# Kernel tuning notes

Measured on AMD Instinct MI355X. Metric: run time of the kernel, lower is better.

## Reference

```python
import jax, jax.numpy as jnp
import numpy as np

VOCAB, EMB, HID, OUT = 128, 128, 256, 2
B, T = 128, 2048


def setup_inputs() -> dict:
    key = jax.random.key(0)
    ks = jax.random.split(key, 8)
    s_ih = 1.0 / np.sqrt(HID)
    inp = {
        "x": jax.random.randint(ks[0], (B, T), 0, VOCAB, dtype=jnp.int32),
        "emb": jax.random.normal(ks[1], (VOCAB, EMB), jnp.float32),
        "W_ih": jax.random.uniform(ks[2], (4 * HID, EMB), jnp.float32, -s_ih, s_ih),
        "W_hh": jax.random.uniform(ks[3], (4 * HID, HID), jnp.float32, -s_ih, s_ih),
        "b_ih": jax.random.uniform(ks[4], (4 * HID,), jnp.float32, -s_ih, s_ih),
        "b_hh": jax.random.uniform(ks[5], (4 * HID,), jnp.float32, -s_ih, s_ih),
        "fc_W": jax.random.normal(ks[6], (OUT, HID), jnp.float32) * np.sqrt(6.0 / (HID + OUT)),
        "fc_b": jnp.zeros((OUT,), jnp.float32),
    }
    return inp


def _lstm_last_hidden(xe, W_ih, W_hh, b_ih, b_hh):
    # xe: [B, T, E]. Precompute all input-to-hidden gate projections (batched GEMM).
    Bsz = xe.shape[0]
    H = W_hh.shape[1]
    xg = jnp.einsum('bte,ge->tbg', xe, W_ih) + (b_ih + b_hh)  # [T, B, 4H]

    def step(carry, xt):
        h, c = carry
        g = xt + h @ W_hh.T                 # [B, 4H]
        i, f, gg, o = jnp.split(g, 4, axis=-1)  # PyTorch gate order i,f,g,o
        i = jax.nn.sigmoid(i)
        f = jax.nn.sigmoid(f)
        gg = jnp.tanh(gg)
        o = jax.nn.sigmoid(o)
        c = f * c + i * gg
        h = o * jnp.tanh(c)
        return (h, c), None

    h0 = jnp.zeros((Bsz, H), xe.dtype)
    c0 = jnp.zeros((Bsz, H), xe.dtype)
    (hT, _), _ = jax.lax.scan(step, (h0, c0), xg)
    return hT  # == output[:, -1, :] for a uni-directional LSTM


def reference(x, emb, W_ih, W_hh, b_ih, b_hh, fc_W, fc_b):
    xe = emb[x]                                   # [B, T, E] embedding lookup
    hT = _lstm_last_hidden(xe, W_ih, W_hh, b_ih, b_hh)
    logits = hT @ fc_W.T + fc_b                   # [B, OUT]
    return logits
```

## Files before the change

### kernel.cpp

```cpp
#include <hip/hip_runtime.h>

#define T_LEN 2048
#define HID   256
#define G4    1024
#define EMBD  128
#define VOCAB 128
#define OUTC  2
#define BSUB  2
#define NWG   64
#define CHK   64
#define XCHS  72
#define HSB   288
#define LOG2E 1.44269504088896340736f

typedef int   i32x4 __attribute__((ext_vector_type(4)));
typedef float f32x4 __attribute__((ext_vector_type(4)));

__device__ __align__(16) float Pbuf[VOCAB * G4];
__device__ __align__(16) signed char Wqb[G4 * HID];
__device__ float Winv[G4];

__global__ void build_P(const float* __restrict__ emb, const float* __restrict__ W_ih,
                        const float* __restrict__ b_ih, const float* __restrict__ b_hh) {
    const int v = blockIdx.x >> 2;
    const int c = ((blockIdx.x & 3) << 8) + threadIdx.x;
    __shared__ float es[EMBD];
    if (threadIdx.x < EMBD) es[threadIdx.x] = emb[v * EMBD + threadIdx.x];
    __syncthreads();
    const float* wr = W_ih + c * EMBD;
    float acc = 0.f;
    #pragma unroll 8
    for (int e = 0; e < EMBD; ++e) acc += es[e] * wr[e];
    const float ks = ((c >> 8) == 2) ? (-2.f * LOG2E) : (-LOG2E);
    const int g  = c >> 8;
    const int rr = c & 255;
    const int wi = rr >> 5;
    const int nt = (rr >> 4) & 1;
    const int l  = rr & 15;
    Pbuf[v * G4 + wi * 128 + nt * 64 + l * 4 + g] = (acc + b_ih[c] + b_hh[c]) * ks;
}

__global__ void quant_W(const float* __restrict__ W_hh) {
    const int row = blockIdx.x;
    const int k   = threadIdx.x;
    __shared__ float red[4];
    const float wv = W_hh[row * HID + k];
    float a = fabsf(wv);
    #pragma unroll
    for (int o = 32; o > 0; o >>= 1) a = fmaxf(a, __shfl_down(a, o, 64));
    if ((k & 63) == 0) red[k >> 6] = a;
    __syncthreads();
    const float m = fmaxf(fmaxf(fmaxf(red[0], red[1]), red[2]), fmaxf(red[3], 1e-30f));
    Wqb[row * HID + k] = (signed char)(int)rintf(wv * (127.f / m));
    const float ks = ((row >> 8) == 2) ? (-2.f * LOG2E) : (-LOG2E);
    if (k == 0) Winv[row] = m * (1.f / (127.f * 127.f)) * ks;
}

__device__ __forceinline__ float sig_p(float p) {
    return __builtin_amdgcn_rcpf(1.f + __builtin_amdgcn_exp2f(p));
}

__global__ __launch_bounds__(512, 2) void lstm_chain(
        const int* __restrict__ x, const float* __restrict__ fc_W,
        const float* __restrict__ fc_b, float* __restrict__ out) {
    __shared__ __align__(16) signed char habuf[2][BSUB * HSB];
    __shared__ int   xch[BSUB * XCHS];
    __shared__ float hfin[BSUB * HID];

    const int tid  = threadIdx.x;
    const int w    = tid >> 6;
    const int lane = tid & 63;
    const int l15  = lane & 15;
    const int quad = lane >> 4;
    const int bbase = blockIdx.x * BSUB;
    const int ub    = w * 32;
    const int bq    = quad >> 1;
    const int ntq   = quad & 1;
    const int colq  = ub + ntq * 16 + l15;

    i32x4 Bf[2][4][4];
    #pragma unroll
    for (int nt = 0; nt < 2; ++nt)
        #pragma unroll
        for (int g = 0; g < 4; ++g) {
            const signed char* wr = Wqb + (size_t)(g * HID + ub + nt * 16 + l15) * HID;
            #pragma unroll
            for (int kt = 0; kt < 4; ++kt)
                Bf[nt][g][kt] = *(const i32x4*)(wr + kt * 64 + quad * 16);
        }
    float winvv[4];
    #pragma unroll
    for (int g = 0; g < 4; ++g) winvv[g] = Winv[g * HID + colq];

    if (tid < BSUB * HSB / 4) ((int*)habuf[0])[tid] = 0;

    float cst = 0.f;
    f32x4 xga, xgb;
    const i32x4 zero4 = {0, 0, 0, 0};
    const float* pbase = Pbuf + w * 128 + ntq * 64 + l15 * 4;
    const signed char* habA = habuf[0] + (l15 >> 3) * HSB + quad * 16;
    const signed char* habB = habuf[1] + (l15 >> 3) * HSB + quad * 16;

#define GATHER(TT, XG)                                                        \
    {                                                                         \
        const int xv = xch[bq * XCHS + (TT)];                                 \
        XG = *(const f32x4*)(pbase + (size_t)xv * G4);                        \
    }

#define STEP(HAB, HN, XC, XN, PF, TT, TCUR)                                   \
    {                                                                         \
        i32x4 af[4];                                                          \
        _Pragma("unroll")                                                     \
        for (int kt = 0; kt < 4; ++kt)                                        \
            af[kt] = *(const i32x4*)((HAB) + kt * 64);                        \
        if (PF) GATHER((TT), XN);                                             \
        i32x4 a0[4], a1[4];                                                   \
        _Pragma("unroll")                                                     \
        for (int g = 0; g < 4; ++g)                                           \
            a0[g] = __builtin_amdgcn_mfma_i32_16x16x64_i8(af[0], Bf[0][g][0], zero4, 0, 0, 0); \
        _Pragma("unroll")                                                     \
        for (int kt = 1; kt < 4; ++kt)                                        \
            _Pragma("unroll")                                                 \
            for (int g = 0; g < 4; ++g)                                       \
                a0[g] = __builtin_amdgcn_mfma_i32_16x16x64_i8(af[kt], Bf[0][g][kt], a0[g], 0, 0, 0); \
        _Pragma("unroll")                                                     \
        for (int g = 0; g < 4; ++g)                                           \
            a1[g] = __builtin_amdgcn_mfma_i32_16x16x64_i8(af[0], Bf[1][g][0], zero4, 0, 0, 0); \
        _Pragma("unroll")                                                     \
        for (int kt = 1; kt < 4; ++kt)                                        \
            _Pragma("unroll")                                                 \
            for (int g = 0; g < 4; ++g)                                       \
                a1[g] = __builtin_amdgcn_mfma_i32_16x16x64_i8(af[kt], Bf[1][g][kt], a1[g], 0, 0, 0); \
                         \
        const int gi_ = ntq ? a1[0][0] : a0[0][0];                            \
        const int gf_ = ntq ? a1[1][0] : a0[1][0];                            \
        const int gg_ = ntq ? a1[2][0] : a0[2][0];                            \
        const int go_ = ntq ? a1[3][0] : a0[3][0];                            \
        const float is = sig_p(fmaf((float)gi_, winvv[0], XC[0]));            \
        const float fs = sig_p(fmaf((float)gf_, winvv[1], XC[1]));            \
        const float gt = fmaf(2.f, sig_p(fmaf((float)gg_, winvv[2], XC[2])), -1.f); \
        const float os = sig_p(fmaf((float)go_, winvv[3], XC[3]));            \
        const float c  = fmaf(fs, cst, is * gt);                              \
        cst = c;                                                              \
        const float hq = fmaf(254.f, sig_p(c * (-2.f * LOG2E)), -127.f) * os; \
        (HN)[bq * HSB + colq] = (signed char)(int)rintf(hq);                  \
        if ((TCUR) == T_LEN - 1) hfin[bq * HID + colq] = hq * (1.f / 127.f);  \
        __syncthreads();                                                      \
    }

    #pragma unroll 1
    for (int ch = 0; ch < T_LEN / CHK; ++ch) {
        if (tid < BSUB * CHK)
            xch[(tid >> 6) * XCHS + (tid & 63)] =
                x[(bbase + (tid >> 6)) * T_LEN + ch * CHK + (tid & 63)];
        __syncthreads();
        GATHER(0, xga);
        const int tb = ch * CHK;
        #pragma unroll 1
        for (int tt = 0; tt < CHK; tt += 2) {
            STEP(habA, habuf[1], xga, xgb, 1, tt + 1, tb + tt);
            STEP(habB, habuf[0], xgb, xga, (tt < CHK - 2), tt + 2, tb + tt + 1);
        }
    }
#undef STEP
#undef GATHER

    if (tid < BSUB * OUTC) {
        const int b = tid >> 1, o = tid & 1;
        float s = fc_b[o];
        #pragma unroll 8
        for (int j = 0; j < HID; ++j) s += hfin[b * HID + j] * fc_W[o * HID + j];
        out[(bbase + b) * OUTC + o] = s;
    }
}

extern "C" void kernel_launch(void* const* d_in, const int* in_sizes, int n_in,
                              void* d_out, int out_size, void* d_ws, size_t ws_size,
                              hipStream_t stream) {
    const int*   x    = (const int*)  d_in[0];
    const float* emb  = (const float*)d_in[1];
    const float* W_ih = (const float*)d_in[2];
    const float* W_hh = (const float*)d_in[3];
    const float* b_ih = (const float*)d_in[4];
    const float* b_hh = (const float*)d_in[5];
    const float* fc_W = (const float*)d_in[6];
    const float* fc_b = (const float*)d_in[7];
    float* out = (float*)d_out;
    (void)d_ws; (void)ws_size;

    build_P<<<dim3(VOCAB * 4), dim3(256), 0, stream>>>(emb, W_ih, b_ih, b_hh);
    quant_W<<<dim3(G4), dim3(HID), 0, stream>>>(W_hh);
    lstm_chain<<<dim3(NWG), dim3(512), 0, stream>>>(x, fc_W, fc_b, out);
}
```

Measured before the change: 1.408 ms.

## Preload full token sequence to LDS and overlap gate math with second MFMA set

Loads each block's whole token sequence (2x2048 ints) into shared memory once at kernel start, removing the per-64-step chunk reloads and their extra barriers. The step now computes gate nonlinearities for the first MFMA tile right after its accumulation, before issuing the second tile's MFMAs, so the transcendental work can overlap MFMA latency. Both tiles' gates are then computed and selected, doubling the activation ALU work per lane and adding register pressure plus 16KB of LDS.

```diff
diff --git a/kernel.cpp b/kernel.cpp
--- a/kernel.cpp
+++ b/kernel.cpp
@@ -8,8 +8,6 @@
 #define OUTC  2
 #define BSUB  2
 #define NWG   64
-#define CHK   64
-#define XCHS  72
 #define HSB   288
 #define LOG2E 1.44269504088896340736f
 
@@ -64,7 +62,7 @@
         const int* __restrict__ x, const float* __restrict__ fc_W,
         const float* __restrict__ fc_b, float* __restrict__ out) {
     __shared__ __align__(16) signed char habuf[2][BSUB * HSB];
-    __shared__ int   xch[BSUB * XCHS];
+    __shared__ __align__(16) int xls[BSUB][T_LEN];
     __shared__ float hfin[BSUB * HID];
 
     const int tid  = threadIdx.x;
@@ -92,6 +90,12 @@
     #pragma unroll
     for (int g = 0; g < 4; ++g) winvv[g] = Winv[g * HID + colq];
 
+    {
+        const i32x4* xsrc = (const i32x4*)(x + (size_t)bbase * T_LEN);
+        i32x4* xdst = (i32x4*)xls;
+        xdst[tid]       = xsrc[tid];
+        xdst[tid + 512] = xsrc[tid + 512];
+    }
     if (tid < BSUB * HSB / 4) ((int*)habuf[0])[tid] = 0;
 
     float cst = 0.f;
@@ -103,7 +107,7 @@
 
 #define GATHER(TT, XG)                                                        \
     {                                                                         \
-        const int xv = xch[bq * XCHS + (TT)];                                 \
+        const int xv = xls[bq][(TT)];                                         \
         XG = *(const f32x4*)(pbase + (size_t)xv * G4);                        \
     }
 
@@ -123,6 +127,12 @@
             _Pragma("unroll")                                                 \
             for (int g = 0; g < 4; ++g)                                       \
                 a0[g] = __builtin_amdgcn_mfma_i32_16x16x64_i8(af[kt], Bf[0][g][kt], a0[g], 0, 0, 0); \
+          \
+        const float i0 = sig_p(fmaf((float)a0[0][0], winvv[0], XC[0]));       \
+        const float f0 = sig_p(fmaf((float)a0[1][0], winvv[1], XC[1]));       \
+        const float g0 = fmaf(2.f, sig_p(fmaf((float)a0[2][0], winvv[2], XC[2])), -1.f); \
+        const float o0 = sig_p(fmaf((float)a0[3][0], winvv[3], XC[3]));       \
+        const float ig0 = i0 * g0;                                            \
         _Pragma("unroll")                                                     \
         for (int g = 0; g < 4; ++g)                                           \
             a1[g] = __builtin_amdgcn_mfma_i32_16x16x64_i8(af[0], Bf[1][g][0], zero4, 0, 0, 0); \
@@ -131,16 +141,16 @@
             _Pragma("unroll")                                                 \
             for (int g = 0; g < 4; ++g)                                       \
                 a1[g] = __builtin_amdgcn_mfma_i32_16x16x64_i8(af[kt], Bf[1][g][kt], a1[g], 0, 0, 0); \
-                         \
-        const int gi_ = ntq ? a1[0][0] : a0[0][0];                            \
-        const int gf_ = ntq ? a1[1][0] : a0[1][0];                            \
-        const int gg_ = ntq ? a1[2][0] : a0[2][0];                            \
-        const int go_ = ntq ? a1[3][0] : a0[3][0];                            \
-        const float is = sig_p(fmaf((float)gi_, winvv[0], XC[0]));            \
-        const float fs = sig_p(fmaf((float)gf_, winvv[1], XC[1]));            \
-        const float gt = fmaf(2.f, sig_p(fmaf((float)gg_, winvv[2], XC[2])), -1.f); \
-        const float os = sig_p(fmaf((float)go_, winvv[3], XC[3]));            \
-        const float c  = fmaf(fs, cst, is * gt);                              \
+        const float i1 = sig_p(fmaf((float)a1[0][0], winvv[0], XC[0]));       \
+        const float f1 = sig_p(fmaf((float)a1[1][0], winvv[1], XC[1]));       \
+        const float g1 = fmaf(2.f, sig_p(fmaf((float)a1[2][0], winvv[2], XC[2])), -1.f); \
+        const float o1 = sig_p(fmaf((float)a1[3][0], winvv[3], XC[3]));       \
+        const float ig1 = i1 * g1;                                            \
+             \
+        const float fs = ntq ? f1 : f0;                                       \
+        const float ig = ntq ? ig1 : ig0;                                     \
+        const float os = ntq ? o1 : o0;                                       \
+        const float c  = fmaf(fs, cst, ig);                                   \
         cst = c;                                                              \
         const float hq = fmaf(254.f, sig_p(c * (-2.f * LOG2E)), -127.f) * os; \
         (HN)[bq * HSB + colq] = (signed char)(int)rintf(hq);                  \
@@ -148,19 +158,12 @@
         __syncthreads();                                                      \
     }
 
+    __syncthreads();
+    GATHER(0, xga);
     #pragma unroll 1
-    for (int ch = 0; ch < T_LEN / CHK; ++ch) {
-        if (tid < BSUB * CHK)
-            xch[(tid >> 6) * XCHS + (tid & 63)] =
-                x[(bbase + (tid >> 6)) * T_LEN + ch * CHK + (tid & 63)];
-        __syncthreads();
-        GATHER(0, xga);
-        const int tb = ch * CHK;
-        #pragma unroll 1
-        for (int tt = 0; tt < CHK; tt += 2) {
-            STEP(habA, habuf[1], xga, xgb, 1, tt + 1, tb + tt);
-            STEP(habB, habuf[0], xgb, xga, (tt < CHK - 2), tt + 2, tb + tt + 1);
-        }
+    for (int tt = 0; tt < T_LEN; tt += 2) {
+        STEP(habA, habuf[1], xga, xgb, 1, tt + 1, tt);
+        STEP(habB, habuf[0], xgb, xga, (tt < T_LEN - 2), tt + 2, tt + 1);
     }
 #undef STEP
 #undef GATHER
```

After: 1.563 ms. 11.0% more time.
